# Optimization experiments

Measured on AMD Instinct MI355X. Metric: run time of the kernel, lower is better.

The kernel has to match this reference:

```python
import jax, jax.numpy as jnp
import numpy as np

N = 100_000      # nodes
E = 800_000      # edges (avg degree 8)
D_IN = 16        # embedding_dimension
H = 128          # hidden_dimension
OUT = 3          # out_dim
NEG_SLOPE = 0.01 # LeakyReLU default


def setup_inputs() -> dict:
    key = jax.random.key(0)
    ks = jax.random.split(key, 9)
    s = 0.05
    return {
        "feature": jax.random.normal(ks[0], (N, D_IN), jnp.float32),
        "edge_index": jax.random.randint(ks[1], (2, E), 0, N, dtype=jnp.int64),
        "edge_type": jax.random.randint(ks[2], (E,), 0, 2, dtype=jnp.int64),
        "W_in": jax.random.normal(ks[3], (D_IN, H), jnp.float32) * s,
        "b_in": jnp.zeros((H,), jnp.float32),
        "W1": jax.random.normal(ks[4], (H, H), jnp.float32) * s,
        "b1": jnp.zeros((H,), jnp.float32),
        "W2": jax.random.normal(ks[5], (H, H), jnp.float32) * s,
        "b2": jnp.zeros((H,), jnp.float32),
        "W_out": jax.random.normal(ks[6], (H, OUT), jnp.float32) * s,
        "b_out": jnp.zeros((OUT,), jnp.float32),
    }


def gcn_conv(x, W, b, src, dst, n):
    """PyG GCNConv: linear -> add self-loops -> D^-1/2 A D^-1/2 aggregation -> bias."""
    h = x @ W                                   # [N, H]
    loop = jnp.arange(n, dtype=src.dtype)
    src_sl = jnp.concatenate([src, loop])       # [E+N]
    dst_sl = jnp.concatenate([dst, loop])
    deg = jax.ops.segment_sum(jnp.ones_like(dst_sl, dtype=h.dtype), dst_sl, num_segments=n)
    dinv = jax.lax.rsqrt(jnp.maximum(deg, 1.0))  # deg >= 1 due to self-loops
    norm = dinv[src_sl] * dinv[dst_sl]          # [E+N]
    msg = h[src_sl] * norm[:, None]             # gather + scale, [E+N, H]
    out = jax.ops.segment_sum(msg, dst_sl, num_segments=n)  # scatter-add
    return out + b


def reference(feature, edge_index, edge_type, W_in, b_in, W1, b1, W2, b2, W_out, b_out):
    # edge_type is accepted but unused, exactly as in the torch forward.
    x = jax.nn.leaky_relu(feature.astype(jnp.float32) @ W_in + b_in, NEG_SLOPE)
    src, dst = edge_index[0], edge_index[1]
    x = gcn_conv(x, W1, b1, src, dst, N)
    # F.dropout with training=False is identity (inference path)
    x = gcn_conv(x, W2, b2, src, dst, N)
    return x @ W_out + b_out
```

## Files before the change

kernel.cpp:

```cpp
#include <hip/hip_runtime.h>
#include <cstdint>

#define DIN 16
#define HD  128
#define RNG 512
#define LB  9
#define MAXB 256
#define CAP 8192
#define PBB 128

static __device__ __forceinline__ void fma4(float4& a, float s, const float4 v) {
    a.x = fmaf(s, v.x, a.x);
    a.y = fmaf(s, v.y, a.y);
    a.z = fmaf(s, v.z, a.z);
    a.w = fmaf(s, v.w, a.w);
}
static __device__ __forceinline__ void add4(float4& a, const float4 v) {
    a.x += v.x; a.y += v.y; a.z += v.z; a.w += v.w;
}
static __device__ __forceinline__ void lrelu4(float4& h) {
    h.x = h.x > 0.f ? h.x : 0.01f * h.x;
    h.y = h.y > 0.f ? h.y : 0.01f * h.y;
    h.z = h.z > 0.f ? h.z : 0.01f * h.z;
    h.w = h.w > 0.f ? h.w : 0.01f * h.w;
}

__global__ __launch_bounds__(256) void k_init(int* __restrict__ binCnt, int R,
                                              const float* __restrict__ W1,
                                              const float* __restrict__ b1,
                                              const float* __restrict__ W2,
                                              const float* __restrict__ b2,
                                              const float* __restrict__ Wout,
                                              const float* __restrict__ bout,
                                              float* __restrict__ Wcp,
                                              float* __restrict__ cbuf) {
    int tid = threadIdx.x;
    for (int i = tid; i < R; i += 256) binCnt[i] = 0;
    __shared__ float sT[HD * 3];
    for (int idx = tid; idx < HD * 3; idx += 256) {
        int k = idx / 3, o = idx - 3 * k;
        float s = 0.f;
        for (int j = 0; j < HD; j++) s = fmaf(W2[k * HD + j], Wout[j * 3 + o], s);
        sT[idx] = s;
    }
    if (tid < 3) {
        float s = bout[tid];
        for (int j = 0; j < HD; j++) s = fmaf(b2[j], Wout[j * 3 + tid], s);
        cbuf[3 + tid] = s;
    }
    __syncthreads();
    if (tid < 3) {
        float s = 0.f;
        for (int j = 0; j < HD; j++) s = fmaf(b1[j], sT[j * 3 + tid], s);
        cbuf[tid] = s;
    }
    for (int idx = tid; idx < HD * 3; idx += 256) {
        int k = idx / 3, o = idx - 3 * k;
        float s = 0.f;
        for (int j = 0; j < HD; j++) s = fmaf(W1[k * HD + j], sT[j * 3 + o], s);
        Wcp[k * 4 + o] = s;
    }
    for (int idx = tid; idx < HD; idx += 256) Wcp[idx * 4 + 3] = 0.f;
}

__global__ __launch_bounds__(1024) void k_front(const int* __restrict__ src,
                                                const int* __restrict__ dst,
                                                int* __restrict__ binCnt,
                                                int* __restrict__ ebin,
                                                int E, int R, int CHK,
                                                const float* __restrict__ F,
                                                const float* __restrict__ Win,
                                                const float* __restrict__ binp,
                                                const float4* __restrict__ Wcp,
                                                float4* __restrict__ Y, int N) {
    int tid = threadIdx.x;
    if (blockIdx.x < PBB) {
        __shared__ int cnt[MAXB];
        __shared__ int rsv[MAXB];
        for (int i = tid; i < R; i += 1024) cnt[i] = 0;
        __syncthreads();
        int e0 = blockIdx.x * CHK;
        int e1 = e0 + CHK; if (e1 > E) e1 = E;
        for (int e = e0 + tid; e < e1; e += 1024) atomicAdd(&cnt[dst[e] >> LB], 1);
        __syncthreads();
        for (int i = tid; i < R; i += 1024) {
            int cc = cnt[i];
            rsv[i] = cc ? atomicAdd(&binCnt[i], cc) : 0;
        }
        __syncthreads();
        for (int i = tid; i < R; i += 1024) cnt[i] = 0;
        __syncthreads();
        for (int e = e0 + tid; e < e1; e += 1024) {
            int s = src[e], d = dst[e];
            int bb = d >> LB;
            int lp = atomicAdd(&cnt[bb], 1);
            ebin[(size_t)bb * CAP + rsv[bb] + lp] = (s << LB) | (d & (RNG - 1));
        }
        return;
    }
    __shared__ float4 sWinT[DIN * HD / 4];
    __shared__ float4 sWcT[HD];
    __shared__ float4 sBin[HD / 4];
    __shared__ float  sF[128 * DIN];
    if (tid < DIN * HD / 4) {
        int k = tid >> 5, rem = tid & 31, l = rem >> 1, c = rem & 1;
        sWinT[k * 32 + c * 16 + l] = ((const float4*)Win)[tid];
    } else if (tid < DIN * HD / 4 + HD) {
        int i = tid - DIN * HD / 4;
        sWcT[(i & 7) * 16 + (i >> 3)] = Wcp[i];
    } else if (tid < DIN * HD / 4 + HD + HD / 4) {
        int i = tid - DIN * HD / 4 - HD;
        sBin[i] = ((const float4*)binp)[i];
    }
    int base = (blockIdx.x - PBB) * 128;
    {
        int n0 = base + (tid >> 4);
        sF[tid] = (n0 < N) ? F[(size_t)base * DIN + tid] : 0.f;
        int n1 = base + ((tid + 1024) >> 4);
        sF[tid + 1024] = (n1 < N) ? F[(size_t)base * DIN + tid + 1024] : 0.f;
    }
    __syncthreads();
    int l = tid & 15;
    int g = tid >> 4;
    int nodeA = base + 2 * g;
    int nodeB = nodeA + 1;
    if (nodeA >= N) return;
    float4 a0 = sBin[l * 2 + 0], a1 = sBin[l * 2 + 1];
    float4 b0 = a0, b1 = a1;
    #pragma unroll
    for (int k = 0; k < DIN; k++) {
        float4 w0 = sWinT[k * 32 + l];
        float4 w1 = sWinT[k * 32 + 16 + l];
        float fA = sF[(2 * g) * DIN + k];
        float fB = sF[(2 * g + 1) * DIN + k];
        fma4(a0, fA, w0); fma4(a1, fA, w1);
        fma4(b0, fB, w0); fma4(b1, fB, w1);
    }
    lrelu4(a0); lrelu4(a1); lrelu4(b0); lrelu4(b1);
    float hA[8] = {a0.x, a0.y, a0.z, a0.w, a1.x, a1.y, a1.z, a1.w};
    float hB[8] = {b0.x, b0.y, b0.z, b0.w, b1.x, b1.y, b1.z, b1.w};
    float pA0 = 0.f, pA1 = 0.f, pA2 = 0.f, pB0 = 0.f, pB1 = 0.f, pB2 = 0.f;
    #pragma unroll
    for (int jj = 0; jj < 8; jj++) {
        float4 wc = sWcT[jj * 16 + l];
        pA0 = fmaf(hA[jj], wc.x, pA0);
        pA1 = fmaf(hA[jj], wc.y, pA1);
        pA2 = fmaf(hA[jj], wc.z, pA2);
        pB0 = fmaf(hB[jj], wc.x, pB0);
        pB1 = fmaf(hB[jj], wc.y, pB1);
        pB2 = fmaf(hB[jj], wc.z, pB2);
    }
    #pragma unroll
    for (int off = 8; off > 0; off >>= 1) {
        pA0 += __shfl_down(pA0, off, 16);
        pA1 += __shfl_down(pA1, off, 16);
        pA2 += __shfl_down(pA2, off, 16);
        pB0 += __shfl_down(pB0, off, 16);
        pB1 += __shfl_down(pB1, off, 16);
        pB2 += __shfl_down(pB2, off, 16);
    }
    if (l == 0) {
        Y[nodeA] = make_float4(pA0, pA1, pA2, 1.0f);
        if (nodeB < N) Y[nodeB] = make_float4(pB0, pB1, pB2, 1.0f);
    }
}

__global__ __launch_bounds__(512) void k_csr(const int* __restrict__ ebin,
                                             const int* __restrict__ binCnt,
                                             const float4* __restrict__ Y,
                                             int* __restrict__ rowptr,
                                             int* __restrict__ ecsr,
                                             float* __restrict__ dinv,
                                             float4* __restrict__ Ys,
                                             int N, int E, int R) {
    __shared__ int c[RNG];
    __shared__ int sb[MAXB];
    __shared__ int swv[8];
    __shared__ int se0;
    int tid = threadIdx.x;
    int b = blockIdx.x;
    c[tid] = 0;
    if (tid < MAXB) sb[tid] = (tid < R) ? binCnt[tid] : 0;
    __syncthreads();
    int cnt = sb[b];
    int part = (tid < b) ? sb[tid] : 0;
    #pragma unroll
    for (int o = 32; o > 0; o >>= 1) part += __shfl_down(part, o, 64);
    if ((tid & 63) == 0) swv[tid >> 6] = part;
    __syncthreads();
    if (tid == 0) {
        int s = 0;
        #pragma unroll
        for (int w = 0; w < 8; w++) s += swv[w];
        se0 = s;
    }
    __syncthreads();
    int e0 = se0;
    int ebase = b * CAP;
    for (int e = tid; e < cnt; e += 512) atomicAdd(&c[ebin[ebase + e] & (RNG - 1)], 1);
    __syncthreads();
    int v0 = c[tid];
    int lane = tid & 63, wid = tid >> 6;
    int sc = v0;
    #pragma unroll
    for (int o = 1; o < 64; o <<= 1) {
        int t = __shfl_up(sc, o, 64);
        if (lane >= o) sc += t;
    }
    if (lane == 63) swv[wid] = sc;
    __syncthreads();
    if (tid < 8) {
        int v = swv[tid];
        int s2 = v;
        #pragma unroll
        for (int o = 1; o < 8; o <<= 1) {
            int t = __shfl_up(s2, o, 8);
            if (tid >= o) s2 += t;
        }
        swv[tid] = s2 - v;
    }
    __syncthreads();
    int excl = sc - v0 + swv[wid];
    int rp0 = e0 + excl;
    int n0 = b * RNG + tid;
    if (n0 <= N) rowptr[n0] = rp0;
    if (n0 < N) {
        float di = rsqrtf((float)v0 + 1.0f);
        dinv[n0] = di;
        float4 y = Y[n0];
        Ys[n0] = make_float4(di * y.x, di * y.y, di * y.z, di);
    }
    c[tid] = rp0;
    __syncthreads();
    for (int e = tid; e < cnt; e += 512) {
        int ed = ebin[ebase + e];
        int pos = atomicAdd(&c[ed & (RNG - 1)], 1);
        ecsr[pos] = ed >> LB;
    }
    if (b == 0 && tid < 16) ecsr[E + tid] = 0;
}

__global__ __launch_bounds__(256) void k_aggA(const int* __restrict__ rowptr,
                                              const int* __restrict__ ecsr,
                                              const float4* __restrict__ Ys,
                                              const float* __restrict__ dinv,
                                              float4* __restrict__ Z1s, int N) {
    int n = blockIdx.x * blockDim.x + threadIdx.x;
    if (n >= N) return;
    int beg = rowptr[n], end = rowptr[n + 1];
    int deg = end - beg;
    float4 acc = Ys[n];
    int4 q0 = *(const int4*)(ecsr + beg);
    int4 q1 = *(const int4*)(ecsr + beg + 4);
    int4 q2 = *(const int4*)(ecsr + beg + 8);
    int si[12] = {q0.x, q0.y, q0.z, q0.w, q1.x, q1.y, q1.z, q1.w,
                  q2.x, q2.y, q2.z, q2.w};
    float4 g[12];
    #pragma unroll
    for (int k = 0; k < 12; k++) g[k] = Ys[si[k]];
    #pragma unroll
    for (int k = 0; k < 12; k++) if (k < deg) add4(acc, g[k]);
    for (int j = beg + 12; j < end; j++) add4(acc, Ys[ecsr[j]]);
    float di = dinv[n];
    float d2 = di * di;
    Z1s[n] = make_float4(d2 * acc.x, d2 * acc.y, d2 * acc.z, d2 * acc.w);
}

__global__ __launch_bounds__(256) void k_aggB(const int* __restrict__ rowptr,
                                              const int* __restrict__ ecsr,
                                              const float4* __restrict__ Z1s,
                                              const float* __restrict__ dinv,
                                              const float* __restrict__ cbuf,
                                              float* __restrict__ out, int N) {
    int n = blockIdx.x * blockDim.x + threadIdx.x;
    if (n >= N) return;
    int beg = rowptr[n], end = rowptr[n + 1];
    int deg = end - beg;
    float4 acc = Z1s[n];
    float di = dinv[n];
    float r = acc.w / di;
    int4 q0 = *(const int4*)(ecsr + beg);
    int4 q1 = *(const int4*)(ecsr + beg + 4);
    int4 q2 = *(const int4*)(ecsr + beg + 8);
    int si[12] = {q0.x, q0.y, q0.z, q0.w, q1.x, q1.y, q1.z, q1.w,
                  q2.x, q2.y, q2.z, q2.w};
    float4 g[12];
    #pragma unroll
    for (int k = 0; k < 12; k++) g[k] = Z1s[si[k]];
    #pragma unroll
    for (int k = 0; k < 12; k++) if (k < deg) add4(acc, g[k]);
    for (int j = beg + 12; j < end; j++) add4(acc, Z1s[ecsr[j]]);
    out[(size_t)n * 3 + 0] = di * acc.x + r * cbuf[0] + cbuf[3];
    out[(size_t)n * 3 + 1] = di * acc.y + r * cbuf[1] + cbuf[4];
    out[(size_t)n * 3 + 2] = di * acc.z + r * cbuf[2] + cbuf[5];
}

extern "C" void kernel_launch(void* const* d_in, const int* in_sizes, int n_in,
                              void* d_out, int out_size, void* d_ws, size_t ws_size,
                              hipStream_t stream) {
    const float* feat = (const float*)d_in[0];
    const int*   ei   = (const int*)d_in[1];
    const float* Win  = (const float*)d_in[3];
    const float* binp = (const float*)d_in[4];
    const float* W1   = (const float*)d_in[5];
    const float* b1   = (const float*)d_in[6];
    const float* W2   = (const float*)d_in[7];
    const float* b2   = (const float*)d_in[8];
    const float* Wout = (const float*)d_in[9];
    const float* bout = (const float*)d_in[10];
    float* out = (float*)d_out;

    int N = in_sizes[0] / DIN;
    int E = in_sizes[2];
    const int* src = ei;
    const int* dst = ei + E;

    int R = (N + RNG - 1) >> LB;
    int CHK = (E + PBB - 1) / PBB;
    int XB = (N + 127) / 128;

    char* p = (char*)d_ws;
    auto alloc = [&](size_t bytes) -> char* {
        char* q = p;
        p += (bytes + 511) & ~(size_t)511;
        return q;
    };
    int*    binCnt = (int*)alloc((size_t)R * 4);
    int*    ebin   = (int*)alloc((size_t)R * CAP * 4);
    int*    ecsr   = (int*)alloc(((size_t)E + 16) * 4);
    int*    rowptr = (int*)alloc((size_t)(N + 1) * 4);
    float4* Y      = (float4*)alloc((size_t)N * 16);
    float4* Ys     = (float4*)alloc((size_t)N * 16);
    float4* Z1s    = (float4*)alloc((size_t)N * 16);
    float*  dinv   = (float*)alloc((size_t)N * 4);
    float*  Wcp    = (float*)alloc(HD * 4 * 4);
    float*  cbuf   = (float*)alloc(8 * 4);

    k_init<<<1, 256, 0, stream>>>(binCnt, R, W1, b1, W2, b2, Wout, bout, Wcp, cbuf);
    k_front<<<PBB + XB, 1024, 0, stream>>>(src, dst, binCnt, ebin, E, R, CHK,
                                           feat, Win, binp, (const float4*)Wcp, Y, N);
    k_csr<<<R, 512, 0, stream>>>(ebin, binCnt, Y, rowptr, ecsr, dinv, Ys, N, E, R);
    k_aggA<<<(N + 255) / 256, 256, 0, stream>>>(rowptr, ecsr, Ys, dinv, Z1s, N);
    k_aggB<<<(N + 255) / 256, 256, 0, stream>>>(rowptr, ecsr, Z1s, dinv, cbuf, out, N);
}
```

Measured before the change: 145.2 us.

## Fuse whole GCN pipeline into one cooperative kernel with grid syncs

Replaces the five-kernel pipeline (init, binned edge partition, CSR build, two aggregations) with a single cooperative kernel of 256 blocks × 1024 threads that uses grid.sync between phases. CSR construction changes from a two-level bin sort to global atomic degree counting, a grid-wide prefix scan and atomic cursor scatter. The folded weight products are now computed redundantly in every block, and a memset is added. The aim is to remove launch gaps and intermediate buffers, at the cost of heavy global atomics, a non-deterministic order of edges within each row, and the expense of grid-wide barriers.

```diff
diff --git a/kernel.cpp b/kernel.cpp
--- a/kernel.cpp
+++ b/kernel.cpp
@@ -1,13 +1,13 @@
 #include <hip/hip_runtime.h>
+#include <hip/hip_cooperative_groups.h>
 #include <cstdint>
+
+namespace cg = cooperative_groups;
 
 #define DIN 16
 #define HD  128
-#define RNG 512
-#define LB  9
-#define MAXB 256
-#define CAP 8192
-#define PBB 128
+#define NB  256
+#define NT  1024
 
 static __device__ __forceinline__ void fma4(float4& a, float s, const float4 v) {
     a.x = fmaf(s, v.x, a.x);
@@ -25,183 +25,133 @@
     h.w = h.w > 0.f ? h.w : 0.01f * h.w;
 }
 
-__global__ __launch_bounds__(256) void k_init(int* __restrict__ binCnt, int R,
-                                              const float* __restrict__ W1,
-                                              const float* __restrict__ b1,
-                                              const float* __restrict__ W2,
-                                              const float* __restrict__ b2,
-                                              const float* __restrict__ Wout,
-                                              const float* __restrict__ bout,
-                                              float* __restrict__ Wcp,
-                                              float* __restrict__ cbuf) {
-    int tid = threadIdx.x;
-    for (int i = tid; i < R; i += 256) binCnt[i] = 0;
-    __shared__ float sT[HD * 3];
-    for (int idx = tid; idx < HD * 3; idx += 256) {
+__global__ __launch_bounds__(NT) void k_fused(
+    const float* __restrict__ F,
+    const int* __restrict__ src, const int* __restrict__ dst,
+    const float* __restrict__ Win, const float* __restrict__ binp,
+    const float* __restrict__ W1, const float* __restrict__ b1,
+    const float* __restrict__ W2, const float* __restrict__ b2,
+    const float* __restrict__ Wout, const float* __restrict__ bout,
+    int* __restrict__ deg, int* __restrict__ cursor, int* __restrict__ ecsr,
+    float4* __restrict__ Y, float4* __restrict__ Ys, float4* __restrict__ Z1s,
+    int* __restrict__ blockSum, float* __restrict__ cbuf,
+    float* __restrict__ out, int N, int E)
+{
+    cg::grid_group grid = cg::this_grid();
+    const int tid  = threadIdx.x;
+    const int bid  = blockIdx.x;
+    const int gtid = bid * NT + tid;
+    const int lane = tid & 63, wid = tid >> 6;
+
+    __shared__ float  sT[HD * 3];
+    __shared__ float4 sWinT[DIN * HD / 4];
+    __shared__ float4 sWcT[HD];
+    __shared__ float4 sBin[HD / 4];
+    __shared__ float  sF[128 * DIN];
+    __shared__ int    swv[16];
+    __shared__ int    sbs[NB];
+    __shared__ int    sbase;
+
+    if (tid < DIN * HD / 4) {
+        int k = tid >> 5, rem = tid & 31, l = rem >> 1, c = rem & 1;
+        sWinT[k * 32 + c * 16 + l] = ((const float4*)Win)[tid];
+    } else if (tid < DIN * HD / 4 + HD / 4) {
+        int i = tid - DIN * HD / 4;
+        sBin[i] = ((const float4*)binp)[i];
+    }
+    for (int e = gtid; e < E; e += NB * NT) atomicAdd(&deg[dst[e]], 1);
+    for (int idx = tid; idx < HD * 3; idx += NT) {
         int k = idx / 3, o = idx - 3 * k;
         float s = 0.f;
         for (int j = 0; j < HD; j++) s = fmaf(W2[k * HD + j], Wout[j * 3 + o], s);
         sT[idx] = s;
     }
-    if (tid < 3) {
-        float s = bout[tid];
-        for (int j = 0; j < HD; j++) s = fmaf(b2[j], Wout[j * 3 + tid], s);
-        cbuf[3 + tid] = s;
-    }
-    __syncthreads();
-    if (tid < 3) {
-        float s = 0.f;
-        for (int j = 0; j < HD; j++) s = fmaf(b1[j], sT[j * 3 + tid], s);
-        cbuf[tid] = s;
-    }
-    for (int idx = tid; idx < HD * 3; idx += 256) {
+    __syncthreads();
+    for (int idx = tid; idx < HD * 3; idx += NT) {
         int k = idx / 3, o = idx - 3 * k;
         float s = 0.f;
         for (int j = 0; j < HD; j++) s = fmaf(W1[k * HD + j], sT[j * 3 + o], s);
-        Wcp[k * 4 + o] = s;
-    }
-    for (int idx = tid; idx < HD; idx += 256) Wcp[idx * 4 + 3] = 0.f;
-}
-
-__global__ __launch_bounds__(1024) void k_front(const int* __restrict__ src,
-                                                const int* __restrict__ dst,
-                                                int* __restrict__ binCnt,
-                                                int* __restrict__ ebin,
-                                                int E, int R, int CHK,
-                                                const float* __restrict__ F,
-                                                const float* __restrict__ Win,
-                                                const float* __restrict__ binp,
-                                                const float4* __restrict__ Wcp,
-                                                float4* __restrict__ Y, int N) {
-    int tid = threadIdx.x;
-    if (blockIdx.x < PBB) {
-        __shared__ int cnt[MAXB];
-        __shared__ int rsv[MAXB];
-        for (int i = tid; i < R; i += 1024) cnt[i] = 0;
-        __syncthreads();
-        int e0 = blockIdx.x * CHK;
-        int e1 = e0 + CHK; if (e1 > E) e1 = E;
-        for (int e = e0 + tid; e < e1; e += 1024) atomicAdd(&cnt[dst[e] >> LB], 1);
-        __syncthreads();
-        for (int i = tid; i < R; i += 1024) {
-            int cc = cnt[i];
-            rsv[i] = cc ? atomicAdd(&binCnt[i], cc) : 0;
+        ((float*)&sWcT[(k & 7) * 16 + (k >> 3)])[o] = s;
+    }
+    for (int k = tid; k < HD; k += NT) ((float*)&sWcT[(k & 7) * 16 + (k >> 3)])[3] = 0.f;
+    if (bid == 0 && tid < 3) {
+        float s2v = bout[tid];
+        for (int j = 0; j < HD; j++) s2v = fmaf(b2[j], Wout[j * 3 + tid], s2v);
+        cbuf[3 + tid] = s2v;
+        float s1 = 0.f;
+        for (int j = 0; j < HD; j++) s1 = fmaf(b1[j], sT[j * 3 + tid], s1);
+        cbuf[tid] = s1;
+    }
+    __syncthreads();
+    int nper = (N + NB - 1) / NB;
+    int nb0 = bid * nper;
+    int nb1 = nb0 + nper; if (nb1 > N) nb1 = N;
+    for (int cb = nb0; cb < nb1; cb += 128) {
+        {
+            int n0 = cb + (tid >> 4);
+            sF[tid] = (n0 < N) ? F[(size_t)cb * DIN + tid] : 0.f;
+            int n1 = cb + ((tid + 1024) >> 4);
+            sF[tid + 1024] = (n1 < N) ? F[(size_t)cb * DIN + tid + 1024] : 0.f;
         }
         __syncthreads();
-        for (int i = tid; i < R; i += 1024) cnt[i] = 0;
+        int l = tid & 15;
+        int g = tid >> 4;
+        int nodeA = cb + 2 * g;
+        int nodeB = nodeA + 1;
+        if (nodeA < nb1) {
+            float4 a0 = sBin[l * 2 + 0], a1 = sBin[l * 2 + 1];
+            float4 b0 = a0, b1v = a1;
+            #pragma unroll
+            for (int k = 0; k < DIN; k++) {
+                float4 w0 = sWinT[k * 32 + l];
+                float4 w1 = sWinT[k * 32 + 16 + l];
+                float fA = sF[(2 * g) * DIN + k];
+                float fB = sF[(2 * g + 1) * DIN + k];
+                fma4(a0, fA, w0); fma4(a1, fA, w1);
+                fma4(b0, fB, w0); fma4(b1v, fB, w1);
+            }
+            lrelu4(a0); lrelu4(a1); lrelu4(b0); lrelu4(b1v);
+            float hA[8] = {a0.x, a0.y, a0.z, a0.w, a1.x, a1.y, a1.z, a1.w};
+            float hB[8] = {b0.x, b0.y, b0.z, b0.w, b1v.x, b1v.y, b1v.z, b1v.w};
+            float pA0 = 0.f, pA1 = 0.f, pA2 = 0.f, pB0 = 0.f, pB1 = 0.f, pB2 = 0.f;
+            #pragma unroll
+            for (int jj = 0; jj < 8; jj++) {
+                float4 wc = sWcT[jj * 16 + l];
+                pA0 = fmaf(hA[jj], wc.x, pA0);
+                pA1 = fmaf(hA[jj], wc.y, pA1);
+                pA2 = fmaf(hA[jj], wc.z, pA2);
+                pB0 = fmaf(hB[jj], wc.x, pB0);
+                pB1 = fmaf(hB[jj], wc.y, pB1);
+                pB2 = fmaf(hB[jj], wc.z, pB2);
+            }
+            #pragma unroll
+            for (int off = 8; off > 0; off >>= 1) {
+                pA0 += __shfl_down(pA0, off, 16);
+                pA1 += __shfl_down(pA1, off, 16);
+                pA2 += __shfl_down(pA2, off, 16);
+                pB0 += __shfl_down(pB0, off, 16);
+                pB1 += __shfl_down(pB1, off, 16);
+                pB2 += __shfl_down(pB2, off, 16);
+            }
+            if (l == 0) {
+                Y[nodeA] = make_float4(pA0, pA1, pA2, 1.0f);
+                if (nodeB < nb1) Y[nodeB] = make_float4(pB0, pB1, pB2, 1.0f);
+            }
+        }
         __syncthreads();
-        for (int e = e0 + tid; e < e1; e += 1024) {
-            int s = src[e], d = dst[e];
-            int bb = d >> LB;
-            int lp = atomicAdd(&cnt[bb], 1);
-            ebin[(size_t)bb * CAP + rsv[bb] + lp] = (s << LB) | (d & (RNG - 1));
-        }
-        return;
-    }
-    __shared__ float4 sWinT[DIN * HD / 4];
-    __shared__ float4 sWcT[HD];
-    __shared__ float4 sBin[HD / 4];
-    __shared__ float  sF[128 * DIN];
-    if (tid < DIN * HD / 4) {
-        int k = tid >> 5, rem = tid & 31, l = rem >> 1, c = rem & 1;
-        sWinT[k * 32 + c * 16 + l] = ((const float4*)Win)[tid];
-    } else if (tid < DIN * HD / 4 + HD) {
-        int i = tid - DIN * HD / 4;
-        sWcT[(i & 7) * 16 + (i >> 3)] = Wcp[i];
-    } else if (tid < DIN * HD / 4 + HD + HD / 4) {
-        int i = tid - DIN * HD / 4 - HD;
-        sBin[i] = ((const float4*)binp)[i];
-    }
-    int base = (blockIdx.x - PBB) * 128;
-    {
-        int n0 = base + (tid >> 4);
-        sF[tid] = (n0 < N) ? F[(size_t)base * DIN + tid] : 0.f;
-        int n1 = base + ((tid + 1024) >> 4);
-        sF[tid + 1024] = (n1 < N) ? F[(size_t)base * DIN + tid + 1024] : 0.f;
-    }
-    __syncthreads();
-    int l = tid & 15;
-    int g = tid >> 4;
-    int nodeA = base + 2 * g;
-    int nodeB = nodeA + 1;
-    if (nodeA >= N) return;
-    float4 a0 = sBin[l * 2 + 0], a1 = sBin[l * 2 + 1];
-    float4 b0 = a0, b1 = a1;
-    #pragma unroll
-    for (int k = 0; k < DIN; k++) {
-        float4 w0 = sWinT[k * 32 + l];
-        float4 w1 = sWinT[k * 32 + 16 + l];
-        float fA = sF[(2 * g) * DIN + k];
-        float fB = sF[(2 * g + 1) * DIN + k];
-        fma4(a0, fA, w0); fma4(a1, fA, w1);
-        fma4(b0, fB, w0); fma4(b1, fB, w1);
-    }
-    lrelu4(a0); lrelu4(a1); lrelu4(b0); lrelu4(b1);
-    float hA[8] = {a0.x, a0.y, a0.z, a0.w, a1.x, a1.y, a1.z, a1.w};
-    float hB[8] = {b0.x, b0.y, b0.z, b0.w, b1.x, b1.y, b1.z, b1.w};
-    float pA0 = 0.f, pA1 = 0.f, pA2 = 0.f, pB0 = 0.f, pB1 = 0.f, pB2 = 0.f;
-    #pragma unroll
-    for (int jj = 0; jj < 8; jj++) {
-        float4 wc = sWcT[jj * 16 + l];
-        pA0 = fmaf(hA[jj], wc.x, pA0);
-        pA1 = fmaf(hA[jj], wc.y, pA1);
-        pA2 = fmaf(hA[jj], wc.z, pA2);
-        pB0 = fmaf(hB[jj], wc.x, pB0);
-        pB1 = fmaf(hB[jj], wc.y, pB1);
-        pB2 = fmaf(hB[jj], wc.z, pB2);
-    }
-    #pragma unroll
-    for (int off = 8; off > 0; off >>= 1) {
-        pA0 += __shfl_down(pA0, off, 16);
-        pA1 += __shfl_down(pA1, off, 16);
-        pA2 += __shfl_down(pA2, off, 16);
-        pB0 += __shfl_down(pB0, off, 16);
-        pB1 += __shfl_down(pB1, off, 16);
-        pB2 += __shfl_down(pB2, off, 16);
-    }
-    if (l == 0) {
-        Y[nodeA] = make_float4(pA0, pA1, pA2, 1.0f);
-        if (nodeB < N) Y[nodeB] = make_float4(pB0, pB1, pB2, 1.0f);
-    }
-}
-
-__global__ __launch_bounds__(512) void k_csr(const int* __restrict__ ebin,
-                                             const int* __restrict__ binCnt,
-                                             const float4* __restrict__ Y,
-                                             int* __restrict__ rowptr,
-                                             int* __restrict__ ecsr,
-                                             float* __restrict__ dinv,
-                                             float4* __restrict__ Ys,
-                                             int N, int E, int R) {
-    __shared__ int c[RNG];
-    __shared__ int sb[MAXB];
-    __shared__ int swv[8];
-    __shared__ int se0;
-    int tid = threadIdx.x;
-    int b = blockIdx.x;
-    c[tid] = 0;
-    if (tid < MAXB) sb[tid] = (tid < R) ? binCnt[tid] : 0;
-    __syncthreads();
-    int cnt = sb[b];
-    int part = (tid < b) ? sb[tid] : 0;
-    #pragma unroll
-    for (int o = 32; o > 0; o >>= 1) part += __shfl_down(part, o, 64);
-    if ((tid & 63) == 0) swv[tid >> 6] = part;
-    __syncthreads();
-    if (tid == 0) {
-        int s = 0;
-        #pragma unroll
-        for (int w = 0; w < 8; w++) s += swv[w];
-        se0 = s;
-    }
-    __syncthreads();
-    int e0 = se0;
-    int ebase = b * CAP;
-    for (int e = tid; e < cnt; e += 512) atomicAdd(&c[ebin[ebase + e] & (RNG - 1)], 1);
-    __syncthreads();
-    int v0 = c[tid];
-    int lane = tid & 63, wid = tid >> 6;
-    int sc = v0;
+    }
+    grid.sync();
+
+    const int n = gtid;
+    int myDeg = 0;
+    float myDi = 0.f;
+    if (n < N) {
+        myDeg = deg[n];
+        myDi = rsqrtf((float)myDeg + 1.0f);
+        float4 y = Y[n];
+        Ys[n] = make_float4(myDi * y.x, myDi * y.y, myDi * y.z, myDi);
+    }
+    int sc = myDeg;
     #pragma unroll
     for (int o = 1; o < 64; o <<= 1) {
         int t = __shfl_up(sc, o, 64);
@@ -209,90 +159,84 @@
     }
     if (lane == 63) swv[wid] = sc;
     __syncthreads();
-    if (tid < 8) {
-        int v = swv[tid];
-        int s2 = v;
-        #pragma unroll
-        for (int o = 1; o < 8; o <<= 1) {
-            int t = __shfl_up(s2, o, 8);
+    if (tid < 16) {
+        int x = swv[tid], s2 = x;
+        #pragma unroll
+        for (int o = 1; o < 16; o <<= 1) {
+            int t = __shfl_up(s2, o, 16);
             if (tid >= o) s2 += t;
         }
-        swv[tid] = s2 - v;
-    }
-    __syncthreads();
-    int excl = sc - v0 + swv[wid];
-    int rp0 = e0 + excl;
-    int n0 = b * RNG + tid;
-    if (n0 <= N) rowptr[n0] = rp0;
-    if (n0 < N) {
-        float di = rsqrtf((float)v0 + 1.0f);
-        dinv[n0] = di;
-        float4 y = Y[n0];
-        Ys[n0] = make_float4(di * y.x, di * y.y, di * y.z, di);
-    }
-    c[tid] = rp0;
-    __syncthreads();
-    for (int e = tid; e < cnt; e += 512) {
-        int ed = ebin[ebase + e];
-        int pos = atomicAdd(&c[ed & (RNG - 1)], 1);
-        ecsr[pos] = ed >> LB;
-    }
-    if (b == 0 && tid < 16) ecsr[E + tid] = 0;
-}
-
-__global__ __launch_bounds__(256) void k_aggA(const int* __restrict__ rowptr,
-                                              const int* __restrict__ ecsr,
-                                              const float4* __restrict__ Ys,
-                                              const float* __restrict__ dinv,
-                                              float4* __restrict__ Z1s, int N) {
-    int n = blockIdx.x * blockDim.x + threadIdx.x;
-    if (n >= N) return;
-    int beg = rowptr[n], end = rowptr[n + 1];
-    int deg = end - beg;
-    float4 acc = Ys[n];
-    int4 q0 = *(const int4*)(ecsr + beg);
-    int4 q1 = *(const int4*)(ecsr + beg + 4);
-    int4 q2 = *(const int4*)(ecsr + beg + 8);
-    int si[12] = {q0.x, q0.y, q0.z, q0.w, q1.x, q1.y, q1.z, q1.w,
-                  q2.x, q2.y, q2.z, q2.w};
-    float4 g[12];
+        swv[tid] = s2 - x;
+        if (tid == 15) blockSum[bid] = s2;
+    }
+    __syncthreads();
+    int myExcl = sc - myDeg + swv[wid];
+    grid.sync();
+
+    if (tid < NB) sbs[tid] = blockSum[tid];
+    __syncthreads();
+    int p = (tid < bid) ? sbs[tid] : 0;
     #pragma unroll
-    for (int k = 0; k < 12; k++) g[k] = Ys[si[k]];
-    #pragma unroll
-    for (int k = 0; k < 12; k++) if (k < deg) add4(acc, g[k]);
-    for (int j = beg + 12; j < end; j++) add4(acc, Ys[ecsr[j]]);
-    float di = dinv[n];
-    float d2 = di * di;
-    Z1s[n] = make_float4(d2 * acc.x, d2 * acc.y, d2 * acc.z, d2 * acc.w);
-}
-
-__global__ __launch_bounds__(256) void k_aggB(const int* __restrict__ rowptr,
-                                              const int* __restrict__ ecsr,
-                                              const float4* __restrict__ Z1s,
-                                              const float* __restrict__ dinv,
-                                              const float* __restrict__ cbuf,
-                                              float* __restrict__ out, int N) {
-    int n = blockIdx.x * blockDim.x + threadIdx.x;
-    if (n >= N) return;
-    int beg = rowptr[n], end = rowptr[n + 1];
-    int deg = end - beg;
-    float4 acc = Z1s[n];
-    float di = dinv[n];
-    float r = acc.w / di;
-    int4 q0 = *(const int4*)(ecsr + beg);
-    int4 q1 = *(const int4*)(ecsr + beg + 4);
-    int4 q2 = *(const int4*)(ecsr + beg + 8);
-    int si[12] = {q0.x, q0.y, q0.z, q0.w, q1.x, q1.y, q1.z, q1.w,
-                  q2.x, q2.y, q2.z, q2.w};
-    float4 g[12];
-    #pragma unroll
-    for (int k = 0; k < 12; k++) g[k] = Z1s[si[k]];
-    #pragma unroll
-    for (int k = 0; k < 12; k++) if (k < deg) add4(acc, g[k]);
-    for (int j = beg + 12; j < end; j++) add4(acc, Z1s[ecsr[j]]);
-    out[(size_t)n * 3 + 0] = di * acc.x + r * cbuf[0] + cbuf[3];
-    out[(size_t)n * 3 + 1] = di * acc.y + r * cbuf[1] + cbuf[4];
-    out[(size_t)n * 3 + 2] = di * acc.z + r * cbuf[2] + cbuf[5];
+    for (int o = 32; o > 0; o >>= 1) p += __shfl_down(p, o, 64);
+    if (lane == 0) swv[wid] = p;
+    __syncthreads();
+    if (tid == 0) {
+        int s = 0;
+        #pragma unroll
+        for (int w = 0; w < 16; w++) s += swv[w];
+        sbase = s;
+    }
+    __syncthreads();
+    const int rp = sbase + myExcl;
+    if (n < N) cursor[n] = rp;
+    grid.sync();
+
+    for (int e = gtid; e < E; e += NB * NT) {
+        int s = src[e], d = dst[e];
+        int pos = atomicAdd(&cursor[d], 1);
+        ecsr[pos] = s;
+    }
+    if (gtid < 16) ecsr[E + gtid] = 0;
+    grid.sync();
+
+    if (n < N) {
+        float4 acc = Ys[n];
+        int4 q0 = *(const int4*)(ecsr + rp);
+        int4 q1 = *(const int4*)(ecsr + rp + 4);
+        int4 q2 = *(const int4*)(ecsr + rp + 8);
+        int si[12] = {q0.x, q0.y, q0.z, q0.w, q1.x, q1.y, q1.z, q1.w,
+                      q2.x, q2.y, q2.z, q2.w};
+        float4 g[12];
+        #pragma unroll
+        for (int k = 0; k < 12; k++) g[k] = Ys[si[k]];
+        #pragma unroll
+        for (int k = 0; k < 12; k++) if (k < myDeg) add4(acc, g[k]);
+        for (int j = rp + 12; j < rp + myDeg; j++) add4(acc, Ys[ecsr[j]]);
+        float d2 = myDi * myDi;
+        Z1s[n] = make_float4(d2 * acc.x, d2 * acc.y, d2 * acc.z, d2 * acc.w);
+    }
+    grid.sync();
+
+    if (n < N) {
+        float4 acc = Z1s[n];
+        float r = acc.w / myDi;
+        int4 q0 = *(const int4*)(ecsr + rp);
+        int4 q1 = *(const int4*)(ecsr + rp + 4);
+        int4 q2 = *(const int4*)(ecsr + rp + 8);
+        int si[12] = {q0.x, q0.y, q0.z, q0.w, q1.x, q1.y, q1.z, q1.w,
+                      q2.x, q2.y, q2.z, q2.w};
+        float4 g[12];
+        #pragma unroll
+        for (int k = 0; k < 12; k++) g[k] = Z1s[si[k]];
+        #pragma unroll
+        for (int k = 0; k < 12; k++) if (k < myDeg) add4(acc, g[k]);
+        for (int j = rp + 12; j < rp + myDeg; j++) add4(acc, Z1s[ecsr[j]]);
+        float c0 = cbuf[0], c1 = cbuf[1], c2 = cbuf[2];
+        float c3 = cbuf[3], c4 = cbuf[4], c5 = cbuf[5];
+        out[(size_t)n * 3 + 0] = myDi * acc.x + r * c0 + c3;
+        out[(size_t)n * 3 + 1] = myDi * acc.y + r * c1 + c4;
+        out[(size_t)n * 3 + 2] = myDi * acc.z + r * c2 + c5;
+    }
 }
 
 extern "C" void kernel_launch(void* const* d_in, const int* in_sizes, int n_in,
@@ -315,31 +259,32 @@
     const int* src = ei;
     const int* dst = ei + E;
 
-    int R = (N + RNG - 1) >> LB;
-    int CHK = (E + PBB - 1) / PBB;
-    int XB = (N + 127) / 128;
-
     char* p = (char*)d_ws;
     auto alloc = [&](size_t bytes) -> char* {
         char* q = p;
         p += (bytes + 511) & ~(size_t)511;
         return q;
     };
-    int*    binCnt = (int*)alloc((size_t)R * 4);
-    int*    ebin   = (int*)alloc((size_t)R * CAP * 4);
-    int*    ecsr   = (int*)alloc(((size_t)E + 16) * 4);
-    int*    rowptr = (int*)alloc((size_t)(N + 1) * 4);
-    float4* Y      = (float4*)alloc((size_t)N * 16);
-    float4* Ys     = (float4*)alloc((size_t)N * 16);
-    float4* Z1s    = (float4*)alloc((size_t)N * 16);
-    float*  dinv   = (float*)alloc((size_t)N * 4);
-    float*  Wcp    = (float*)alloc(HD * 4 * 4);
-    float*  cbuf   = (float*)alloc(8 * 4);
-
-    k_init<<<1, 256, 0, stream>>>(binCnt, R, W1, b1, W2, b2, Wout, bout, Wcp, cbuf);
-    k_front<<<PBB + XB, 1024, 0, stream>>>(src, dst, binCnt, ebin, E, R, CHK,
-                                           feat, Win, binp, (const float4*)Wcp, Y, N);
-    k_csr<<<R, 512, 0, stream>>>(ebin, binCnt, Y, rowptr, ecsr, dinv, Ys, N, E, R);
-    k_aggA<<<(N + 255) / 256, 256, 0, stream>>>(rowptr, ecsr, Ys, dinv, Z1s, N);
-    k_aggB<<<(N + 255) / 256, 256, 0, stream>>>(rowptr, ecsr, Z1s, dinv, cbuf, out, N);
-}
+    int*    deg      = (int*)alloc((size_t)N * 4);
+    int*    cursor   = (int*)alloc((size_t)N * 4);
+    int*    ecsr     = (int*)alloc(((size_t)E + 16) * 4);
+    float4* Y        = (float4*)alloc((size_t)N * 16);
+    float4* Ys       = (float4*)alloc((size_t)N * 16);
+    float4* Z1s      = (float4*)alloc((size_t)N * 16);
+    int*    blockSum = (int*)alloc((size_t)NB * 4);
+    float*  cbuf     = (float*)alloc(8 * 4);
+
+    hipMemsetAsync(deg, 0, (size_t)N * 4, stream);
+
+    void* args[] = {
+        (void*)&feat, (void*)&src, (void*)&dst,
+        (void*)&Win, (void*)&binp, (void*)&W1, (void*)&b1,
+        (void*)&W2, (void*)&b2, (void*)&Wout, (void*)&bout,
+        (void*)&deg, (void*)&cursor, (void*)&ecsr,
+        (void*)&Y, (void*)&Ys, (void*)&Z1s,
+        (void*)&blockSum, (void*)&cbuf,
+        (void*)&out, (void*)&N, (void*)&E,
+    };
+    hipLaunchCooperativeKernel((const void*)k_fused, dim3(NB), dim3(NT),
+                               args, 0, stream);
+}
```

Result: slower. 378.5 us (+160.7%).
